# Kernel tuning notes

Measured on AMD Instinct MI355X. Metric: run time of the kernel, lower is better.

Reference implementation:

```python
import jax, jax.numpy as jnp
import numpy as np

DIM = 3            # point feature dim (xyz)
POS_HID = 64       # pos_mlp hidden
ATTN_HID = DIM * 4 # attn_mlp hidden (mult=4)
N_NBR = 16         # points per group
GROUPS = 512       # groups per batch element
MLP_D = N_NBR * DIM  # 48


def setup_inputs() -> dict:
    key = jax.random.key(0)
    ks = jax.random.split(key, 20)
    B = 32
    s = lambda *sh: 1.0 / np.sqrt(sh[0])
    inp = {
        "original_points": jax.random.normal(ks[0], (B, GROUPS, DIM), jnp.float32),
        "data": jax.random.normal(ks[1], (B, GROUPS, N_NBR, DIM), jnp.float32),
        # PointTransformerLayer params
        "w_qkv": jax.random.normal(ks[2], (DIM, DIM * 3), jnp.float32) * s(DIM),
        "pos_w1": jax.random.normal(ks[3], (3, POS_HID), jnp.float32) * s(3),
        "pos_b1": jnp.zeros((POS_HID,), jnp.float32),
        "pos_w2": jax.random.normal(ks[4], (POS_HID, DIM), jnp.float32) * s(POS_HID),
        "pos_b2": jnp.zeros((DIM,), jnp.float32),
        "attn_w1": jax.random.normal(ks[5], (DIM, ATTN_HID), jnp.float32) * s(DIM),
        "attn_b1": jnp.zeros((ATTN_HID,), jnp.float32),
        "attn_w2": jax.random.normal(ks[6], (ATTN_HID, DIM), jnp.float32) * s(ATTN_HID),
        "attn_b2": jnp.zeros((DIM,), jnp.float32),
        # downstream MLP params
        "mlp_w1": jax.random.normal(ks[7], (MLP_D, MLP_D), jnp.float32) * s(MLP_D),
        "mlp_b1": jnp.zeros((MLP_D,), jnp.float32),
        "mlp_w2": jax.random.normal(ks[8], (MLP_D, MLP_D), jnp.float32) * s(MLP_D),
        "mlp_b2": jnp.zeros((MLP_D,), jnp.float32),
        "mlp_w3": jax.random.normal(ks[9], (MLP_D, 1), jnp.float32) * s(MLP_D),
        "mlp_b3": jnp.zeros((1,), jnp.float32),
    }
    return inp


def reference(original_points, data, w_qkv, pos_w1, pos_b1, pos_w2, pos_b2,
              attn_w1, attn_b1, attn_w2, attn_b2,
              mlp_w1, mlp_b1, mlp_w2, mlp_b2, mlp_w3, mlp_b3):
    B, G, n, d = data.shape
    x = data.reshape(B * G, n, d)          # (BG, n, 3)
    pos = x[:, :, :3]                       # pos == features here (f=3)

    # Point-transformer vector attention
    qkv = x @ w_qkv                          # (BG, n, 9)
    q, k, v = jnp.split(qkv, 3, axis=-1)
    rel_pos = pos[:, :, None, :] - pos[:, None, :, :]              # (BG, n, n, 3)
    rel_emb = jax.nn.relu(rel_pos @ pos_w1 + pos_b1) @ pos_w2 + pos_b2  # (BG, n, n, 3)
    qk_rel = q[:, :, None, :] - k[:, None, :, :]                   # (BG, n, n, 3)
    v_ij = v[:, None, :, :] + rel_emb                              # (BG, n, n, 3)
    sim = jax.nn.relu((qk_rel + rel_emb) @ attn_w1 + attn_b1) @ attn_w2 + attn_b2
    attn = jax.nn.softmax(sim, axis=-2)                            # softmax over j
    agg = jnp.einsum('bijd,bijd->bid', attn, v_ij)                 # (BG, n, 3)

    # regroup into (B, 512, 48) exactly as stack(split(512, dim=0))
    sa = agg.reshape(B, G, n * d)
    h = jax.nn.relu(sa @ mlp_w1 + mlp_b1)
    h = jax.nn.relu(h @ mlp_w2 + mlp_b2)
    return h @ mlp_w3 + mlp_b3              # (B, 512, 1)
```

## Files before the change

### kernel.cpp

```cpp
#include <hip/hip_runtime.h>


typedef _Float16 h2 __attribute__((ext_vector_type(2)));
typedef _Float16 h8 __attribute__((ext_vector_type(8)));
typedef float f32x4 __attribute__((ext_vector_type(4)));

#define AH_STRIDE 36
#define MW1_OFF  256
#define MW2_OFF 1408
#define AW2T_OFF 2560

union H8U { h8 v; h2 p[4]; unsigned u[4]; };

__device__ __forceinline__ h2 pkrtz(float a, float b) {
    return __builtin_bit_cast(h2, __builtin_amdgcn_cvt_pkrtz(a, b));
}
__device__ __forceinline__ h2 uash2(unsigned u) {
    return __builtin_bit_cast(h2, u);
}
__device__ __forceinline__ h2 hmax2(h2 a, h2 b) {
    return __builtin_elementwise_max(a, b);
}

#if __has_builtin(__builtin_amdgcn_fdot2)
__device__ __forceinline__ float dot2acc(h2 a, h2 b, float c) {
    return __builtin_amdgcn_fdot2(a, b, c, false);
}
#else
__device__ __forceinline__ float dot2acc(h2 a, h2 b, float c) {
    float d;
    asm("v_dot2_f32_f16 %0, %1, %2, %3"
        : "=v"(d)
        : "v"(__builtin_bit_cast(int, a)), "v"(__builtin_bit_cast(int, b)), "v"(c));
    return d;
}
#endif

__device__ __forceinline__ float dpp_add16(float x) {
    float s = x;
    int t;
    t = __builtin_amdgcn_update_dpp(0, __builtin_bit_cast(int, s), 0x121, 0xf, 0xf, false);
    s += __builtin_bit_cast(float, t);
    t = __builtin_amdgcn_update_dpp(0, __builtin_bit_cast(int, s), 0x122, 0xf, 0xf, false);
    s += __builtin_bit_cast(float, t);
    t = __builtin_amdgcn_update_dpp(0, __builtin_bit_cast(int, s), 0x124, 0xf, 0xf, false);
    s += __builtin_bit_cast(float, t);
    t = __builtin_amdgcn_update_dpp(0, __builtin_bit_cast(int, s), 0x128, 0xf, 0xf, false);
    s += __builtin_bit_cast(float, t);
    return s;
}

__global__ void wpack(const float* __restrict__ pw2, const float* __restrict__ aw1,
                      const float* __restrict__ ab1, const float* __restrict__ aw2,
                      const float* __restrict__ mw1, const float* __restrict__ mw2,
                      unsigned* __restrict__ ws) {
    const int t = threadIdx.x;
    const float L2E = 1.44269504f;
    if (blockIdx.x == 0) {
        if (t < 96) {
            const int hp = t & 31, c = t >> 5;
            ws[c*32+hp] = __builtin_bit_cast(unsigned, pkrtz(pw2[(2*hp)*3+c], pw2[(2*hp+1)*3+c]));
        } else if (t < 114) {
            const int idx = t - 96, r = idx / 6, gp = idx % 6;
            ws[96+r*6+gp] = __builtin_bit_cast(unsigned, pkrtz(aw1[r*12+2*gp], aw1[r*12+2*gp+1]));
        } else if (t < 120) {
            const int gp = t - 114;
            ws[114+gp] = __builtin_bit_cast(unsigned, pkrtz(ab1[2*gp], ab1[2*gp+1]));
        } else if (t < 138) {
            const int idx = t - 120, gp = idx / 3, c = idx % 3;
            ws[120+gp*3+c] = __builtin_bit_cast(unsigned,
                pkrtz(aw2[(2*gp)*3+c] * L2E, aw2[(2*gp+1)*3+c] * L2E));
        }
    }
    const int idx = blockIdx.x * 256 + t;
    if (idx < 1152) {
        const int cp = idx / 48, o = idx % 48;
        ws[MW1_OFF + idx] = __builtin_bit_cast(unsigned,
            pkrtz(mw1[(2*cp)*48+o], mw1[(2*cp+1)*48+o]));
        ws[MW2_OFF + idx] = __builtin_bit_cast(unsigned,
            pkrtz(mw2[(2*cp)*48+o], mw2[(2*cp+1)*48+o]));
    }
    if (idx < 512) {
        const int ch = idx >> 8, rem = idx & 255;
        const int l = rem >> 2, d = rem & 3;
        const int c = (l & 15) & 3;
        const bool valid = c < 3;
        const int h0 = ((l >> 4) * 8) + 2*d + 32*ch;
        const float v0 = valid ? pw2[h0*3 + c] : 0.0f;
        const float v1 = valid ? pw2[(h0+1)*3 + c] : 0.0f;
        ws[AW2T_OFF + idx] = __builtin_bit_cast(unsigned, pkrtz(v0, v1));
    }
}

struct SmWave {
    float q4[64], k4[64], v4[64];
    float sa[48], h1[48];
    unsigned a1h[16 * AH_STRIDE];
    unsigned a2h[16 * AH_STRIDE];
};

__global__ __launch_bounds__(256, 6) void pt_main(
    const float* __restrict__ data,
    const float* __restrict__ wqkv,
    const float* __restrict__ pw1,
    const float* __restrict__ pb1,
    const float* __restrict__ pb2,
    const float* __restrict__ ab2,
    const float* __restrict__ mb1,
    const float* __restrict__ mb2,
    const float* __restrict__ mw3,
    const float* __restrict__ mb3,
    const unsigned* __restrict__ wsp,
    float* __restrict__ out)
{
    __shared__ __attribute__((aligned(16))) SmWave sm[4];

    const int tid = threadIdx.x;
    const int w   = tid >> 6;
    const int ln  = tid & 63;
    const int g   = blockIdx.x * 4 + w;
    SmWave& S = sm[w];

    const int p  = ln & 15;
    const float x0 = data[g*48 + p*3 + 0];
    const float x1 = data[g*48 + p*3 + 1];
    const float x2 = data[g*48 + p*3 + 2];

    if (ln < 48) {
        const int sec = ln >> 4;
        float* dst = (sec == 0) ? S.q4 : (sec == 1) ? S.k4 : S.v4;
        #pragma unroll
        for (int c = 0; c < 3; ++c) {
            dst[p*4+c] = fmaf(x0, wqkv[0*9 + sec*3 + c],
                         fmaf(x1, wqkv[1*9 + sec*3 + c],
                         x2 * wqkv[2*9 + sec*3 + c]));
        }
        dst[p*4+3] = 0.0f;
    }

    {
        const int qd = ln >> 4;
        const int hc = qd << 4;
        float s[16];
        #pragma unroll
        for (int c = 0; c < 16; ++c) {
            const int h = hc + c;
            s[c] = fmaf(x0, pw1[h], fmaf(x1, pw1[64+h], x2 * pw1[128+h]));
        }
        uint4 a1u0, a1u1, a2u0, a2u1;
        #pragma unroll
        for (int d = 0; d < 4; ++d) {
            const int c = d * 2;
            (&a1u0.x)[d] = __builtin_bit_cast(unsigned, pkrtz(s[c]   + pb1[hc+c],   s[c+1] + pb1[hc+c+1]));
            (&a1u1.x)[d] = __builtin_bit_cast(unsigned, pkrtz(s[8+c] + pb1[hc+8+c], s[9+c] + pb1[hc+9+c]));
            (&a2u0.x)[d] = __builtin_bit_cast(unsigned, pkrtz(s[c],   s[c+1]));
            (&a2u1.x)[d] = __builtin_bit_cast(unsigned, pkrtz(s[8+c], s[9+c]));
        }
        const int base = p * AH_STRIDE + (qd << 3);
        *(uint4*)&S.a1h[base]     = a1u0;
        *(uint4*)&S.a1h[base + 4] = a1u1;
        *(uint4*)&S.a2h[base]     = a2u0;
        *(uint4*)&S.a2h[base + 4] = a2u1;
    }
    __builtin_amdgcn_wave_barrier();

    const int j = p, q = ln >> 4;
    const float4 kv = *(const float4*)&S.k4[j*4];
    const float4 vv = *(const float4*)&S.v4[j*4];
    const h2 z2 = {(_Float16)0, (_Float16)0};
    const float L2E = 1.44269504f;
    const float mb_0 = ab2[0] * L2E, mb_1 = ab2[1] * L2E, mb_2 = ab2[2] * L2E;

    H8U af0, af1;
    *(uint4*)&af0 = *(const uint4*)&wsp[AW2T_OFF + ln*4];
    *(uint4*)&af1 = *(const uint4*)&wsp[AW2T_OFF + 256 + ln*4];
    H8U b2c0, b2c1;
    b2c0.v = *(const h8*)&S.a2h[j * AH_STRIDE + q*4];
    b2c1.v = *(const h8*)&S.a2h[j * AH_STRIDE + q*4 + 16];

    const f32x4 pb2v = {pb2[0], pb2[1], pb2[2], 0.0f};
    float e[4][3];
    #pragma unroll
    for (int s = 0; s < 4; ++s) { e[s][0] = 0.f; e[s][1] = 0.f; e[s][2] = 0.f; }

    #pragma unroll
    for (int t = 0; t < 16; ++t) {
        H8U r0, r1, d0, d1;
        r0.v = *(const h8*)&S.a1h[t * AH_STRIDE + q*4];
        r1.v = *(const h8*)&S.a1h[t * AH_STRIDE + q*4 + 16];
        #pragma unroll
        for (int m = 0; m < 4; ++m) {
            d0.p[m] = hmax2(r0.p[m] - b2c0.p[m], z2);
            d1.p[m] = hmax2(r1.p[m] - b2c1.p[m], z2);
        }
        f32x4 acc = __builtin_amdgcn_mfma_f32_16x16x32_f16(af0.v, d0.v, pb2v, 0, 0, 0);
        acc = __builtin_amdgcn_mfma_f32_16x16x32_f16(af1.v, d1.v, acc, 0, 0, 0);
        const int s = t >> 2;
        const bool keep = (q == (t & 3));
        e[s][0] = keep ? acc[0] : e[s][0];
        e[s][1] = keep ? acc[1] : e[s][1];
        e[s][2] = keep ? acc[2] : e[s][2];
    }

    #pragma unroll
    for (int half = 0; half < 2; ++half) {
        const int iA = q + 8*half, iB = iA + 4;
        const int ha = 2*half, hb = 2*half + 1;

        const float eA0 = e[ha][0], eA1 = e[ha][1], eA2 = e[ha][2];
        const float eB0 = e[hb][0], eB1 = e[hb][1], eB2 = e[hb][2];

        const float4 qA = *(const float4*)&S.q4[iA*4];
        const float4 qB = *(const float4*)&S.q4[iB*4];

        const float viA0 = vv.x + eA0, viA1 = vv.y + eA1, viA2 = vv.z + eA2;
        const float viB0 = vv.x + eB0, viB1 = vv.y + eB1, viB2 = vv.z + eB2;
        const float siA0 = qA.x - kv.x + eA0, siA1 = qA.y - kv.y + eA1, siA2 = qA.z - kv.z + eA2;
        const float siB0 = qB.x - kv.x + eB0, siB1 = qB.y - kv.y + eB1, siB2 = qB.z - kv.z + eB2;

        const h2 sAx = pkrtz(siA0, siA0), sAy = pkrtz(siA1, siA1), sAz = pkrtz(siA2, siA2);
        const h2 sBx = pkrtz(siB0, siB0), sBy = pkrtz(siB1, siB1), sBz = pkrtz(siB2, siB2);
        float mA0 = mb_0, mA1 = mb_1, mA2 = mb_2;
        float mB0 = mb_0, mB1 = mb_1, mB2 = mb_2;
        #pragma unroll
        for (int gp = 0; gp < 6; ++gp) {
            const h2 b1p = uash2(wsp[114+gp]);
            const h2 u0 = uash2(wsp[96+0*6+gp]);
            const h2 u1 = uash2(wsp[96+1*6+gp]);
            const h2 u2 = uash2(wsp[96+2*6+gp]);
            const h2 v0 = uash2(wsp[120+gp*3+0]);
            const h2 v1 = uash2(wsp[120+gp*3+1]);
            const h2 v2 = uash2(wsp[120+gp*3+2]);
            h2 accA = b1p, accB = b1p;
            accA = __builtin_elementwise_fma(sAx, u0, accA);
            accA = __builtin_elementwise_fma(sAy, u1, accA);
            accA = __builtin_elementwise_fma(sAz, u2, accA);
            accB = __builtin_elementwise_fma(sBx, u0, accB);
            accB = __builtin_elementwise_fma(sBy, u1, accB);
            accB = __builtin_elementwise_fma(sBz, u2, accB);
            h2 hA = hmax2(accA, z2), hB = hmax2(accB, z2);
            mA0 = dot2acc(hA, v0, mA0);
            mA1 = dot2acc(hA, v1, mA1);
            mA2 = dot2acc(hA, v2, mA2);
            mB0 = dot2acc(hB, v0, mB0);
            mB1 = dot2acc(hB, v1, mB1);
            mB2 = dot2acc(hB, v2, mB2);
        }

        const float pA0 = __builtin_amdgcn_exp2f(mA0);
        const float pA1 = __builtin_amdgcn_exp2f(mA1);
        const float pA2 = __builtin_amdgcn_exp2f(mA2);
        const float pB0 = __builtin_amdgcn_exp2f(mB0);
        const float pB1 = __builtin_amdgcn_exp2f(mB1);
        const float pB2 = __builtin_amdgcn_exp2f(mB2);

        const float nA0 = dpp_add16(pA0 * viA0);
        const float nA1 = dpp_add16(pA1 * viA1);
        const float nA2 = dpp_add16(pA2 * viA2);
        const float dA0 = dpp_add16(pA0);
        const float dA1 = dpp_add16(pA1);
        const float dA2 = dpp_add16(pA2);
        const float nB0 = dpp_add16(pB0 * viB0);
        const float nB1 = dpp_add16(pB1 * viB1);
        const float nB2 = dpp_add16(pB2 * viB2);
        const float dB0 = dpp_add16(pB0);
        const float dB1 = dpp_add16(pB1);
        const float dB2 = dpp_add16(pB2);

        if (j == 0) {
            S.sa[iA*3+0] = nA0 * __builtin_amdgcn_rcpf(dA0);
            S.sa[iA*3+1] = nA1 * __builtin_amdgcn_rcpf(dA1);
            S.sa[iA*3+2] = nA2 * __builtin_amdgcn_rcpf(dA2);
            S.sa[iB*3+0] = nB0 * __builtin_amdgcn_rcpf(dB0);
            S.sa[iB*3+1] = nB1 * __builtin_amdgcn_rcpf(dB1);
            S.sa[iB*3+2] = nB2 * __builtin_amdgcn_rcpf(dB2);
        }
    }
    __builtin_amdgcn_wave_barrier();

    if (ln < 48) {
        const int o = ln;
        float a0 = 0.f, a1 = 0.f;
        #pragma unroll
        for (int c = 0; c < 48; c += 4) {
            const float4 sa = *(const float4*)&S.sa[c];
            const h2 pa = pkrtz(sa.x, sa.y);
            const h2 pb = pkrtz(sa.z, sa.w);
            a0 = dot2acc(pa, uash2(wsp[MW1_OFF + (c>>1)*48 + o]), a0);
            a1 = dot2acc(pb, uash2(wsp[MW1_OFF + ((c>>1)+1)*48 + o]), a1);
        }
        S.h1[o] = fmaxf(a0 + a1 + mb1[o], 0.0f);
        __builtin_amdgcn_wave_barrier();
        float b0 = 0.f, b1 = 0.f;
        #pragma unroll
        for (int c = 0; c < 48; c += 4) {
            const float4 hh = *(const float4*)&S.h1[c];
            const h2 pa = pkrtz(hh.x, hh.y);
            const h2 pb = pkrtz(hh.z, hh.w);
            b0 = dot2acc(pa, uash2(wsp[MW2_OFF + (c>>1)*48 + o]), b0);
            b1 = dot2acc(pb, uash2(wsp[MW2_OFF + ((c>>1)+1)*48 + o]), b1);
        }
        const float h2v = fmaxf(b0 + b1 + mb2[o], 0.0f);
        const float fv = h2v * mw3[o];
        const float r = dpp_add16(fv);
        const int ri = __builtin_bit_cast(int, r);
        const float tot =
            __builtin_bit_cast(float, __builtin_amdgcn_readlane(ri, 0)) +
            __builtin_bit_cast(float, __builtin_amdgcn_readlane(ri, 16)) +
            __builtin_bit_cast(float, __builtin_amdgcn_readlane(ri, 32));
        if (o == 0) out[g] = tot + mb3[0];
    }
}

extern "C" void kernel_launch(void* const* d_in, const int* in_sizes, int n_in,
                              void* d_out, int out_size, void* d_ws, size_t ws_size,
                              hipStream_t stream) {
    const float* data = (const float*)d_in[1];
    unsigned* ws = (unsigned*)d_ws;
    const int groups = out_size;

    wpack<<<5, 256, 0, stream>>>(
        (const float*)d_in[5],
        (const float*)d_in[7],
        (const float*)d_in[8],
        (const float*)d_in[9],
        (const float*)d_in[11],
        (const float*)d_in[13],
        ws);

    pt_main<<<groups / 4, 256, 0, stream>>>(
        data,
        (const float*)d_in[2],
        (const float*)d_in[3],
        (const float*)d_in[4],
        (const float*)d_in[6],
        (const float*)d_in[10],
        (const float*)d_in[12],
        (const float*)d_in[14],
        (const float*)d_in[15],
        (const float*)d_in[16],
        ws,
        (float*)d_out);
}
```

Before: 127.3 us.

## Use block-diagonal pos_w2 MFMA weights so each result accumulates rows directly

The rel-pos MLP second layer now uses eight pre-packed block-diagonal A fragments. Each of the four MFMA output rows picks up only its own query row's hidden units, so four t-steps sum into one accumulator and the per-lane select logic goes away. This removes discarded MFMA output and the masking, but loads A fragments from global/workspace inside the loop. The pos_w1 and pos_b1 loads are also vectorised to float4, and the wpack grid grows to fill the larger packed table.

```diff
diff --git a/kernel.cpp b/kernel.cpp
--- a/kernel.cpp
+++ b/kernel.cpp
@@ -80,14 +80,16 @@
         ws[MW2_OFF + idx] = __builtin_bit_cast(unsigned,
             pkrtz(mw2[(2*cp)*48+o], mw2[(2*cp+1)*48+o]));
     }
-    if (idx < 512) {
-        const int ch = idx >> 8, rem = idx & 255;
+    if (idx < 2048) {
+        const int m = idx >> 8, rem = idx & 255;
         const int l = rem >> 2, d = rem & 3;
-        const int c = (l & 15) & 3;
-        const bool valid = c < 3;
-        const int h0 = ((l >> 4) * 8) + 2*d + 32*ch;
-        const float v0 = valid ? pw2[h0*3 + c] : 0.0f;
-        const float v1 = valid ? pw2[(h0+1)*3 + c] : 0.0f;
+        const int row = l & 15, c = row & 3, u = row >> 2;
+        const int kloc = ((l >> 4) * 8) + 2*d;
+        const int kg = 32*m + kloc;
+        const int up = kg >> 6, h = kg & 63;
+        const bool valid = (c < 3) && (u == up);
+        const float v0 = valid ? pw2[h*3 + c] : 0.0f;
+        const float v1 = valid ? pw2[(h+1)*3 + c] : 0.0f;
         ws[AW2T_OFF + idx] = __builtin_bit_cast(unsigned, pkrtz(v0, v1));
     }
 }
@@ -143,16 +145,34 @@
         const int hc = qd << 4;
         float s[16];
         #pragma unroll
-        for (int c = 0; c < 16; ++c) {
-            const int h = hc + c;
-            s[c] = fmaf(x0, pw1[h], fmaf(x1, pw1[64+h], x2 * pw1[128+h]));
+        for (int wv = 0; wv < 4; ++wv) {
+            const float4 r0 = *(const float4*)&pw1[hc + 4*wv];
+            const float4 r1 = *(const float4*)&pw1[64 + hc + 4*wv];
+            const float4 r2 = *(const float4*)&pw1[128 + hc + 4*wv];
+            #pragma unroll
+            for (int cc = 0; cc < 4; ++cc) {
+                const int c = wv*4 + cc;
+                s[c] = fmaf(x0, (&r0.x)[cc], fmaf(x1, (&r1.x)[cc], x2 * (&r2.x)[cc]));
+            }
+        }
+        const float4 b0 = *(const float4*)&pb1[hc];
+        const float4 b1 = *(const float4*)&pb1[hc + 4];
+        const float4 b2 = *(const float4*)&pb1[hc + 8];
+        const float4 b3 = *(const float4*)&pb1[hc + 12];
+        float bb[16];
+        #pragma unroll
+        for (int cc = 0; cc < 4; ++cc) {
+            bb[cc]    = (&b0.x)[cc];
+            bb[4+cc]  = (&b1.x)[cc];
+            bb[8+cc]  = (&b2.x)[cc];
+            bb[12+cc] = (&b3.x)[cc];
         }
         uint4 a1u0, a1u1, a2u0, a2u1;
         #pragma unroll
         for (int d = 0; d < 4; ++d) {
             const int c = d * 2;
-            (&a1u0.x)[d] = __builtin_bit_cast(unsigned, pkrtz(s[c]   + pb1[hc+c],   s[c+1] + pb1[hc+c+1]));
-            (&a1u1.x)[d] = __builtin_bit_cast(unsigned, pkrtz(s[8+c] + pb1[hc+8+c], s[9+c] + pb1[hc+9+c]));
+            (&a1u0.x)[d] = __builtin_bit_cast(unsigned, pkrtz(s[c]   + bb[c],   s[c+1] + bb[c+1]));
+            (&a1u1.x)[d] = __builtin_bit_cast(unsigned, pkrtz(s[8+c] + bb[8+c], s[9+c] + bb[9+c]));
             (&a2u0.x)[d] = __builtin_bit_cast(unsigned, pkrtz(s[c],   s[c+1]));
             (&a2u1.x)[d] = __builtin_bit_cast(unsigned, pkrtz(s[8+c], s[9+c]));
         }
@@ -171,35 +191,34 @@
     const float L2E = 1.44269504f;
     const float mb_0 = ab2[0] * L2E, mb_1 = ab2[1] * L2E, mb_2 = ab2[2] * L2E;
 
-    H8U af0, af1;
-    *(uint4*)&af0 = *(const uint4*)&wsp[AW2T_OFF + ln*4];
-    *(uint4*)&af1 = *(const uint4*)&wsp[AW2T_OFF + 256 + ln*4];
     H8U b2c0, b2c1;
     b2c0.v = *(const h8*)&S.a2h[j * AH_STRIDE + q*4];
     b2c1.v = *(const h8*)&S.a2h[j * AH_STRIDE + q*4 + 16];
 
     const f32x4 pb2v = {pb2[0], pb2[1], pb2[2], 0.0f};
+    const unsigned* afb = wsp + AW2T_OFF + ln*4;
+
     float e[4][3];
     #pragma unroll
-    for (int s = 0; s < 4; ++s) { e[s][0] = 0.f; e[s][1] = 0.f; e[s][2] = 0.f; }
-
-    #pragma unroll
-    for (int t = 0; t < 16; ++t) {
-        H8U r0, r1, d0, d1;
-        r0.v = *(const h8*)&S.a1h[t * AH_STRIDE + q*4];
-        r1.v = *(const h8*)&S.a1h[t * AH_STRIDE + q*4 + 16];
-        #pragma unroll
-        for (int m = 0; m < 4; ++m) {
-            d0.p[m] = hmax2(r0.p[m] - b2c0.p[m], z2);
-            d1.p[m] = hmax2(r1.p[m] - b2c1.p[m], z2);
-        }
-        f32x4 acc = __builtin_amdgcn_mfma_f32_16x16x32_f16(af0.v, d0.v, pb2v, 0, 0, 0);
-        acc = __builtin_amdgcn_mfma_f32_16x16x32_f16(af1.v, d1.v, acc, 0, 0, 0);
-        const int s = t >> 2;
-        const bool keep = (q == (t & 3));
-        e[s][0] = keep ? acc[0] : e[s][0];
-        e[s][1] = keep ? acc[1] : e[s][1];
-        e[s][2] = keep ? acc[2] : e[s][2];
+    for (int s = 0; s < 4; ++s) {
+        f32x4 acc = pb2v;
+        #pragma unroll
+        for (int tt = 0; tt < 4; ++tt) {
+            const int t = 4*s + tt;
+            H8U r0, r1, d0, d1, afa, afc;
+            r0.v = *(const h8*)&S.a1h[t * AH_STRIDE + q*4];
+            r1.v = *(const h8*)&S.a1h[t * AH_STRIDE + q*4 + 16];
+            *(uint4*)&afa = *(const uint4*)&afb[(2*tt)   * 256];
+            *(uint4*)&afc = *(const uint4*)&afb[(2*tt+1) * 256];
+            #pragma unroll
+            for (int m = 0; m < 4; ++m) {
+                d0.p[m] = hmax2(r0.p[m] - b2c0.p[m], z2);
+                d1.p[m] = hmax2(r1.p[m] - b2c1.p[m], z2);
+            }
+            acc = __builtin_amdgcn_mfma_f32_16x16x32_f16(afa.v, d0.v, acc, 0, 0, 0);
+            acc = __builtin_amdgcn_mfma_f32_16x16x32_f16(afc.v, d1.v, acc, 0, 0, 0);
+        }
+        e[s][0] = acc[0]; e[s][1] = acc[1]; e[s][2] = acc[2];
     }
 
     #pragma unroll
@@ -319,7 +338,7 @@
     unsigned* ws = (unsigned*)d_ws;
     const int groups = out_size;
 
-    wpack<<<5, 256, 0, stream>>>(
+    wpack<<<8, 256, 0, stream>>>(
         (const float*)d_in[5],
         (const float*)d_in[7],
         (const float*)d_in[8],
```

Result: no change. 128.0 us (+0.5%).
